# Kernel tuning notes

Measured on AMD Instinct MI355X. Metric: run time of the kernel, lower is better.

Reference implementation:

```python
import jax, jax.numpy as jnp
import numpy as np

IN_FEATS, N_HIDDEN, NUM_LAYERS, N_CLASSES, CLS_HIDDEN = 166, 76, 2, 2, 510
T, N, E = 3, 100000, 1600000
RRELU_SLOPE = (1.0 / 8.0 + 1.0 / 3.0) / 2.0  # eval-mode RReLU = leaky relu with mean slope


def setup_inputs() -> dict:
    key = jax.random.key(0)
    ks = jax.random.split(key, 24)
    d = {}
    d['feats'] = jax.random.normal(ks[0], (T, N, IN_FEATS), jnp.float32)
    d['src'] = jax.random.randint(ks[1], (T, E), 0, N, jnp.int32)
    d['dst'] = jax.random.randint(ks[2], (T, E), 0, N, jnp.int32)
    # TopK scorers (uniform +-1/sqrt(feats))
    s0 = 1.0 / np.sqrt(IN_FEATS)
    s1 = 1.0 / np.sqrt(N_HIDDEN)
    d['scorer0'] = jax.random.uniform(ks[3], (IN_FEATS, 1), jnp.float32, -s0, s0)
    d['scorer1'] = jax.random.uniform(ks[4], (N_HIDDEN, 1), jnp.float32, -s1, s1)
    # GCN weights (xavier-ish)
    d['gcn_w0'] = jax.random.normal(ks[5], (IN_FEATS, N_HIDDEN), jnp.float32) * np.sqrt(2.0 / (IN_FEATS + N_HIDDEN))
    d['gcn_w1'] = jax.random.normal(ks[6], (N_HIDDEN, N_HIDDEN), jnp.float32) * np.sqrt(2.0 / (2 * N_HIDDEN))
    # GRU params, torch layout: W_ih [3H, H_in], W_hh [3H, H], gate order (r, z, n)
    g = 1.0 / np.sqrt(N_HIDDEN)
    H3 = 3 * N_HIDDEN
    d['gru0_wih'] = jax.random.uniform(ks[7], (H3, N_HIDDEN), jnp.float32, -g, g)
    d['gru0_whh'] = jax.random.uniform(ks[8], (H3, N_HIDDEN), jnp.float32, -g, g)
    d['gru0_bih'] = jax.random.uniform(ks[9], (H3,), jnp.float32, -g, g)
    d['gru0_bhh'] = jax.random.uniform(ks[10], (H3,), jnp.float32, -g, g)
    d['gru1_wih'] = jax.random.uniform(ks[11], (H3, N_HIDDEN), jnp.float32, -g, g)
    d['gru1_whh'] = jax.random.uniform(ks[12], (H3, N_HIDDEN), jnp.float32, -g, g)
    d['gru1_bih'] = jax.random.uniform(ks[13], (H3,), jnp.float32, -g, g)
    d['gru1_bhh'] = jax.random.uniform(ks[14], (H3,), jnp.float32, -g, g)
    # MLP
    m1 = 1.0 / np.sqrt(N_HIDDEN)
    m2 = 1.0 / np.sqrt(CLS_HIDDEN)
    d['mlp_w1'] = jax.random.uniform(ks[15], (N_HIDDEN, CLS_HIDDEN), jnp.float32, -m1, m1)
    d['mlp_b1'] = jax.random.uniform(ks[16], (CLS_HIDDEN,), jnp.float32, -m1, m1)
    d['mlp_w2'] = jax.random.uniform(ks[17], (CLS_HIDDEN, N_CLASSES), jnp.float32, -m2, m2)
    d['mlp_b2'] = jax.random.uniform(ks[18], (N_CLASSES,), jnp.float32, -m2, m2)
    return d


def _topk_pool(x, scorer, k):
    # x: [N, F]; returns X_tilde: [F, k]
    scores = (x @ scorer).ravel() / jnp.linalg.norm(scorer)
    vals, idx = jax.lax.top_k(scores, k)
    out = x[idx] * jnp.tanh(vals)[:, None]  # [k, F]
    return out.T


def _gru_step(x, h, wih, whh, bih, bhh):
    # x: [B, H_in], h: [B, H]; torch GRU gate order r, z, n
    gx = x @ wih.T + bih
    gh = h @ whh.T + bhh
    H = h.shape[1]
    rx, zx, nx = gx[:, :H], gx[:, H:2 * H], gx[:, 2 * H:]
    rh, zh, nh = gh[:, :H], gh[:, H:2 * H], gh[:, 2 * H:]
    r = jax.nn.sigmoid(rx + rh)
    z = jax.nn.sigmoid(zx + zh)
    n = jnp.tanh(nx + r * nh)
    return (1.0 - z) * n + z * h


def _graph_conv(x, W, src, dst, n_nodes):
    # DGL GraphConv, norm='both', bias=False, RReLU (eval) activation
    deg_out = jnp.zeros((n_nodes,), x.dtype).at[src].add(1.0)
    deg_in = jnp.zeros((n_nodes,), x.dtype).at[dst].add(1.0)
    norm_src = jnp.clip(deg_out, 1.0, None) ** -0.5
    norm_dst = jnp.clip(deg_in, 1.0, None) ** -0.5
    h = (x * norm_src[:, None]) @ W  # project first (small out dim)
    agg = jax.ops.segment_sum(h[src], dst, num_segments=n_nodes)
    out = agg * norm_dst[:, None]
    return jnp.where(out >= 0, out, out * RRELU_SLOPE)


def reference(feats, src, dst, scorer0, scorer1, gcn_w0, gcn_w1,
              gru0_wih, gru0_whh, gru0_bih, gru0_bhh,
              gru1_wih, gru1_whh, gru1_bih, gru1_bhh,
              mlp_w1, mlp_b1, mlp_w2, mlp_b2):
    scorers = [scorer0, scorer1]
    gcn_ws = [gcn_w0, gcn_w1]
    grus = [(gru0_wih, gru0_whh, gru0_bih, gru0_bhh),
            (gru1_wih, gru1_whh, gru1_bih, gru1_bhh)]
    feat_list = [feats[t] for t in range(T)]
    for i in range(NUM_LAYERS):
        W = gcn_ws[i]
        wih, whh, bih, bhh = grus[i]
        for t in range(T):
            x_tilde = _topk_pool(feat_list[t], scorers[i], N_HIDDEN)  # [F, k]
            W = _gru_step(x_tilde, W, wih, whh, bih, bhh)  # evolve weights
            feat_list[t] = _graph_conv(feat_list[t], W, src[t], dst[t], N)
    h = feat_list[-1]
    h = jax.nn.relu(h @ mlp_w1 + mlp_b1)
    return h @ mlp_w2 + mlp_b2
```

## Files before the change

### kernel.cpp

```cpp
#include <hip/hip_runtime.h>
#include <math.h>

#define NN 100000
#define EE 1600000
#define F0 166
#define HID 76
#define H3 228
#define CHID 510
#define SLOPE 0.22916666666666666f
#define CAND_MAX 4096
#define NBIN 4096
#define HPAD 20

#define BSH 9
#define BSZ 512
#define NBKT 196
#define CH 4096
#define NCHK 391
#define NBAND 13
#define AGG_NWG 7422

__device__ __forceinline__ unsigned f2key(float f){
    unsigned u = __float_as_uint(f);
    return (u & 0x80000000u) ? ~u : (u | 0x80000000u);
}
__device__ __forceinline__ float key2f(unsigned k){
    unsigned u = (k & 0x80000000u) ? (k & 0x7fffffffu) : ~k;
    return __uint_as_float(u);
}

__global__ void scorer_norms_k(const float* __restrict__ s0, const float* __restrict__ s1,
                               float* __restrict__ outn){
    __shared__ float red[256];
    int tid = threadIdx.x;
    float a = 0.f;
    for (int k = tid; k < F0; k += 256) a += s0[k]*s0[k];
    red[tid] = a; __syncthreads();
    for (int s = 128; s > 0; s >>= 1){ if (tid < s) red[tid] += red[tid+s]; __syncthreads(); }
    if (tid == 0) outn[0] = 1.0f/sqrtf(red[0]);
    __syncthreads();
    float b = 0.f;
    for (int k = tid; k < HID; k += 256) b += s1[k]*s1[k];
    red[tid] = b; __syncthreads();
    for (int s = 128; s > 0; s >>= 1){ if (tid < s) red[tid] += red[tid+s]; __syncthreads(); }
    if (tid == 0) outn[1] = 1.0f/sqrtf(red[0]);
}

__global__ void pad_k(const float* __restrict__ w1, const float* __restrict__ b1,
                      const float* __restrict__ w2, float* __restrict__ w1t,
                      float* __restrict__ b1p, float* __restrict__ w2p){
    int idx = blockIdx.x*256 + threadIdx.x;
    if (idx < 512*HID){
        int j = idx / HID, k = idx - j*HID;
        w1t[idx] = (j < CHID) ? w1[k*CHID + j] : 0.f;
    }
    if (idx < 512)  b1p[idx] = (idx < CHID)   ? b1[idx] : 0.f;
    if (idx < 1024) w2p[idx] = (idx < CHID*2) ? w2[idx] : 0.f;
}


__global__ __launch_bounds__(256) void p1_hist_k(const int* __restrict__ src, const int* __restrict__ dst,
                                                 int* __restrict__ bhS, int* __restrict__ bhD){
    __shared__ int hS[NBKT], hD[NBKT];
    int t = blockIdx.y, blk = blockIdx.x, tid = threadIdx.x;
    for (int i = tid; i < NBKT; i += 256){ hS[i] = 0; hD[i] = 0; }
    __syncthreads();
    size_t ebase = (size_t)t*EE + (size_t)blk*CH;
    int m = EE - blk*CH; if (m > CH) m = CH;
    for (int j = tid; j < m; j += 256){
        atomicAdd(&hS[src[ebase + j] >> BSH], 1);
        atomicAdd(&hD[dst[ebase + j] >> BSH], 1);
    }
    __syncthreads();
    for (int i = tid; i < NBKT; i += 256){
        bhS[((size_t)t*NBKT + i)*NCHK + blk] = hS[i];
        bhD[((size_t)t*NBKT + i)*NCHK + blk] = hD[i];
    }
}

__global__ __launch_bounds__(512) void p2_scan_k(int* __restrict__ bhS, int* __restrict__ bhD,
                                                 int* __restrict__ ctS, int* __restrict__ ctD){
    __shared__ int sd[512];
    int b = blockIdx.x, t = blockIdx.y, tid = threadIdx.x;
    for (int a = 0; a < 2; a++){
        int* bh = a ? bhD : bhS;
        int* ct = a ? ctD : ctS;
        int* row = bh + ((size_t)t*NBKT + b)*NCHK;
        int v = (tid < NCHK) ? row[tid] : 0;
        sd[tid] = v; __syncthreads();
        for (int off = 1; off < 512; off <<= 1){
            int x = (tid >= off) ? sd[tid - off] : 0;
            __syncthreads();
            sd[tid] += x;
            __syncthreads();
        }
        if (tid < NCHK) row[tid] = sd[tid] - v;
        if (tid == 511) ct[t*NBKT + b] = sd[511];
        __syncthreads();
    }
}

__global__ __launch_bounds__(256) void p3_base_k(const int* __restrict__ ctS, const int* __restrict__ ctD,
                                                 int* __restrict__ bbS, int* __restrict__ bbD){
    __shared__ int sd[256];
    int tid = threadIdx.x;
    for (int a = 0; a < 2; a++){
        const int* ct = a ? ctD : ctS;
        int* bb = a ? bbD : bbS;
        for (int t = 0; t < 3; t++){
            int v = (tid < NBKT) ? ct[t*NBKT + tid] : 0;
            sd[tid] = v; __syncthreads();
            for (int off = 1; off < 256; off <<= 1){
                int x = (tid >= off) ? sd[tid - off] : 0;
                __syncthreads();
                sd[tid] += x;
                __syncthreads();
            }
            if (tid < NBKT) bb[t*(NBKT+1) + tid] = sd[tid] - v;
            if (tid == 0)   bb[t*(NBKT+1) + NBKT] = EE;
            __syncthreads();
        }
    }
}

__global__ __launch_bounds__(256) void p4_scatter_k(const int* __restrict__ src, const int* __restrict__ dst,
                                                    const int* __restrict__ bhS, const int* __restrict__ bhD,
                                                    const int* __restrict__ bbS, const int* __restrict__ bbD,
                                                    int* __restrict__ srcpart,
                                                    unsigned* __restrict__ pairpart){
    __shared__ int baseS[NBKT], baseD[NBKT], cS[NBKT], cD[NBKT];
    int t = blockIdx.y, blk = blockIdx.x, tid = threadIdx.x;
    for (int i = tid; i < NBKT; i += 256){
        baseS[i] = bbS[t*(NBKT+1) + i] + bhS[((size_t)t*NBKT + i)*NCHK + blk];
        baseD[i] = bbD[t*(NBKT+1) + i] + bhD[((size_t)t*NBKT + i)*NCHK + blk];
        cS[i] = 0; cD[i] = 0;
    }
    __syncthreads();
    size_t ebase = (size_t)t*EE + (size_t)blk*CH;
    int m = EE - blk*CH; if (m > CH) m = CH;
    int* sp = srcpart + (size_t)t*EE;
    unsigned* pp = pairpart + (size_t)t*EE;
    for (int j = tid; j < m; j += 256){
        int s = src[ebase + j], d = dst[ebase + j];
        int bs = s >> BSH, bd = d >> BSH;
        int r0 = atomicAdd(&cS[bs], 1);
        sp[baseS[bs] + r0] = s;
        int r1 = atomicAdd(&cD[bd], 1);
        pp[baseD[bd] + r1] = ((unsigned)s << BSH) | (unsigned)(d & (BSZ-1));
    }
}

__global__ __launch_bounds__(256) void p5_degO_k(const int* __restrict__ srcpart,
                                                 const int* __restrict__ bbS,
                                                 float* __restrict__ nO){
    __shared__ int cnt[BSZ];
    int b = blockIdx.x, t = blockIdx.y, tid = threadIdx.x;
    for (int i = tid; i < BSZ; i += 256) cnt[i] = 0;
    __syncthreads();
    int st = bbS[t*(NBKT+1) + b], en = bbS[t*(NBKT+1) + b + 1];
    const int* sp = srcpart + (size_t)t*EE;
    for (int j = st + tid; j < en; j += 256) atomicAdd(&cnt[sp[j] & (BSZ-1)], 1);
    __syncthreads();
    int nb = b << BSH;
    for (int i = tid; i < BSZ; i += 256){
        int n = nb + i;
        if (n < NN){
            int o = cnt[i]; if (o < 1) o = 1;
            nO[t*NN + n] = 1.0f/sqrtf((float)o);
        }
    }
}

__global__ __launch_bounds__(512) void p6_csr_k(const unsigned* __restrict__ pairpart,
                                                const int* __restrict__ bbD,
                                                int* __restrict__ degI, int* __restrict__ rs,
                                                float* __restrict__ nI,
                                                int* __restrict__ col){
    __shared__ int cnt2[BSZ*NBAND];
    __shared__ int fc2[BSZ*NBAND];
    __shared__ int sd[BSZ];
    int b = blockIdx.x, t = blockIdx.y, tid = threadIdx.x;
    for (int i = tid; i < BSZ*NBAND; i += 512){ cnt2[i] = 0; fc2[i] = 0; }
    __syncthreads();
    int st = bbD[t*(NBKT+1) + b], en = bbD[t*(NBKT+1) + b + 1];
    const unsigned* pp = pairpart + (size_t)t*EE;
    for (int j = st + tid; j < en; j += 512){
        unsigned p = pp[j];
        int li   = (int)(p & (BSZ-1));
        int band = (int)(p >> (BSH + 13));
        atomicAdd(&cnt2[li*NBAND + band], 1);
    }
    __syncthreads();
    int rowcnt = 0;
    #pragma unroll
    for (int bb = 0; bb < NBAND; bb++) rowcnt += cnt2[tid*NBAND + bb];
    sd[tid] = rowcnt; __syncthreads();
    for (int off = 1; off < 512; off <<= 1){
        int x = (tid >= off) ? sd[tid - off] : 0;
        __syncthreads();
        sd[tid] += x;
        __syncthreads();
    }
    int rowEx = sd[tid] - rowcnt;
    int run = rowEx;
    #pragma unroll
    for (int bb = 0; bb < NBAND; bb++){
        int cvv = cnt2[tid*NBAND + bb];
        cnt2[tid*NBAND + bb] = run;
        run += cvv;
    }
    int nb = b << BSH;
    int n = nb + tid;
    if (n < NN){
        degI[t*NN + n] = rowcnt;
        rs[t*NN + n] = st + rowEx;
        int ii = rowcnt; if (ii < 1) ii = 1;
        nI[t*NN + n] = 1.0f/sqrtf((float)ii);
    }
    __syncthreads();
    int* ct = col + (size_t)t*EE;
    for (int j = st + tid; j < en; j += 512){
        unsigned p = pp[j];
        int s  = (int)(p >> BSH);
        int li = (int)(p & (BSZ-1));
        int band = s >> 13;
        int r = atomicAdd(&fc2[li*NBAND + band], 1);
        ct[st + cnt2[li*NBAND + band] + r] = s;
    }
}


template<int F, int PAD>
__global__ __launch_bounds__(256) void score_k(const float* __restrict__ x,
                                               const float* __restrict__ scorer,
                                               const float* __restrict__ invn,
                                               float* __restrict__ scores,
                                               unsigned* hist){
    __shared__ float xs[64*PAD];
    __shared__ float part[256];
    int tid = threadIdx.x;
    int n0 = blockIdx.x*64;
    int nodes = NN - n0; if (nodes > 64) nodes = 64;
    for (int idx = tid; idx < nodes*F; idx += 256){
        int n = idx / F, k = idx - n*F;
        xs[n*PAD + k] = x[(size_t)(n0+n)*F + k];
    }
    __syncthreads();
    int w = __builtin_amdgcn_readfirstlane(tid >> 6);
    int lane = tid & 63;
    int k0 = (F*w) >> 2, k1 = (F*(w+1)) >> 2;
    const float* xrow = xs + lane*PAD;
    float s = 0.f;
    for (int k = k0; k < k1; k++) s += xrow[k]*scorer[k];
    part[w*64 + lane] = s;
    __syncthreads();
    if (tid < 64 && n0 + tid < NN){
        float tot = (part[tid] + part[64+tid] + part[128+tid] + part[192+tid]) * invn[0];
        scores[n0 + tid] = tot;
        atomicAdd(&hist[f2key(tot) >> 20], 1u);
    }
}

__global__ __launch_bounds__(256) void compact_k(const float* __restrict__ scores,
                                                 const unsigned* __restrict__ hist,
                                                 float* __restrict__ cv, int* __restrict__ ci, int* cnt){
    __shared__ unsigned cs[256];
    __shared__ int thr_s;
    int tid = threadIdx.x;
    unsigned s = 0;
    int base = NBIN - 1 - tid*16;
    for (int j = 0; j < 16; j++) s += hist[base - j];
    cs[tid] = s; __syncthreads();
    if (tid == 0){
        unsigned acc = 0; int c = 0;
        for (; c < 256; c++){ if (acc + cs[c] >= 76u) break; acc += cs[c]; }
        int b = NBIN - 1 - c*16;
        int sel = 0;
        for (int j = 0; j < 16; j++){
            acc += hist[b - j];
            if (acc >= 76u){ sel = b - j; break; }
        }
        thr_s = sel;
    }
    __syncthreads();
    int thr = thr_s;
    int n = blockIdx.x*256 + tid;
    if (n >= NN) return;
    float sv = scores[n];
    if ((int)(f2key(sv) >> 20) >= thr){
        int p = atomicAdd(cnt, 1);
        if (p < CAND_MAX){ cv[p] = sv; ci[p] = n; }
    }
}

__global__ __launch_bounds__(256) void topk_k(const float* __restrict__ cv,
                                              const int* __restrict__ ci,
                                              const int* __restrict__ cnt,
                                              int* __restrict__ topidx,
                                              float* __restrict__ tanhv){
    __shared__ unsigned long long keys[CAND_MAX];
    int tid = threadIdx.x;
    int M = *cnt; if (M > CAND_MAX) M = CAND_MAX;
    for (int i = tid; i < M; i += 256)
        keys[i] = ((unsigned long long)f2key(cv[i]) << 32) | (unsigned)(~ci[i]);
    __syncthreads();
    for (int i = tid; i < M; i += 256){
        unsigned long long ki = keys[i];
        int r = 0;
        for (int j = 0; j < M; j++) r += (keys[j] > ki) ? 1 : 0;
        if (r < 76){
            topidx[r] = (int)(~(unsigned)(ki & 0xffffffffu));
            tanhv[r]  = tanhf(key2f((unsigned)(ki >> 32)));
        }
    }
}

template<int F>
__global__ void gru_k(const float* __restrict__ cur, const int* __restrict__ topidx,
                      const float* __restrict__ tanhv, float* __restrict__ W,
                      float* __restrict__ Wt,
                      const float* __restrict__ wih, const float* __restrict__ whh,
                      const float* __restrict__ bih, const float* __restrict__ bhh){
    __shared__ float xr[HID], hr[HID], gx[H3], gh[H3];
    int r = blockIdx.x, tid = threadIdx.x;
    if (tid < HID){
        xr[tid] = cur[(size_t)topidx[tid]*F + r] * tanhv[tid];
        hr[tid] = W[r*HID + tid];
    }
    __syncthreads();
    if (tid < H3){
        const float* wi = wih + tid*HID;
        const float* wh = whh + tid*HID;
        float sa = 0.f, sb = 0.f;
        for (int k = 0; k < HID; k++){ sa += xr[k]*wi[k]; sb += hr[k]*wh[k]; }
        gx[tid] = bih[tid] + sa;
        gh[tid] = bhh[tid] + sb;
    }
    __syncthreads();
    if (tid < HID){
        float rr = 1.f/(1.f + expf(-(gx[tid] + gh[tid])));
        float zz = 1.f/(1.f + expf(-(gx[HID+tid] + gh[HID+tid])));
        float nn = tanhf(gx[2*HID+tid] + rr*gh[2*HID+tid]);
        float nv = (1.f - zz)*nn + zz*hr[tid];
        W[r*HID + tid] = nv;
        int c = tid >> 2, i = tid & 3;
        Wt[(c*F + r)*4 + i] = nv;
    }
}

template<int F, int PAD, int NB>
__global__ __launch_bounds__(256) void gemm_k(const float* __restrict__ x,
                                              const float* __restrict__ Wt,
                                              const float* __restrict__ nO,
                                              float* __restrict__ h){
    __shared__ __align__(16) float xs[NB*PAD];
    int tid = threadIdx.x;
    int n0 = blockIdx.x*NB;
    int nodes = NN - n0; if (nodes > NB) nodes = NB;
    for (int idx = tid; idx < nodes*F; idx += 256){
        int n = idx / F, k = idx - n*F;
        xs[n*PAD + k] = x[(size_t)(n0+n)*F + k];
    }
    __syncthreads();
    int w = __builtin_amdgcn_readfirstlane(tid >> 6);
    int lane = tid & 63;
    int c0 = w*5;
    const float4* Wt4 = (const float4*)Wt;
    float4 accA[5], accB[5];
    #pragma unroll
    for (int c = 0; c < 5; c++){
        accA[c] = make_float4(0.f,0.f,0.f,0.f);
        accB[c] = make_float4(0.f,0.f,0.f,0.f);
    }
    const float* xA = xs + lane*PAD;
    const float* xB = xs + ((NB==128) ? (lane+64)*PAD : lane*PAD);
    for (int k = 0; k < F; k++){
        float xa = xA[k];
        float xb = 0.f;
        if constexpr (NB == 128) xb = xB[k];
        #pragma unroll
        for (int c = 0; c < 5; c++){
            float4 wv = Wt4[(c0 + c)*F + k];
            accA[c].x += xa*wv.x; accA[c].y += xa*wv.y;
            accA[c].z += xa*wv.z; accA[c].w += xa*wv.w;
            if constexpr (NB == 128){
                accB[c].x += xb*wv.x; accB[c].y += xb*wv.y;
                accB[c].z += xb*wv.z; accB[c].w += xb*wv.w;
            }
        }
    }
    int nc = (w == 3) ? 4 : 5;
    int nA = n0 + lane;
    if (nA < NN){
        float nm = nO[nA];
        float4* h4 = (float4*)h + (size_t)nA*HPAD + c0;
        for (int c = 0; c < nc; c++){
            float4 a = accA[c];
            h4[c] = make_float4(a.x*nm, a.y*nm, a.z*nm, a.w*nm);
        }
    }
    if constexpr (NB == 128){
        int nB = n0 + 64 + lane;
        if (nB < NN){
            float nm = nO[nB];
            float4* h4 = (float4*)h + (size_t)nB*HPAD + c0;
            for (int c = 0; c < nc; c++){
                float4 a = accB[c];
                h4[c] = make_float4(a.x*nm, a.y*nm, a.z*nm, a.w*nm);
            }
        }
    }
}

__global__ __launch_bounds__(256) void agg_k(const int* __restrict__ rs, const int* __restrict__ degI,
                      const int* __restrict__ col, const float* __restrict__ h,
                      const float* __restrict__ nI, float* __restrict__ ft){
    int b0 = blockIdx.x;
    int xcd = b0 & 7, i0 = b0 >> 3;
    const int q = AGG_NWG >> 3;
    const int r8 = AGG_NWG & 7;
    int bs = (xcd < r8) ? (xcd*(q+1) + i0) : (r8*(q+1) + (xcd - r8)*q + i0);
    int idx = bs*256 + threadIdx.x;
    if (idx >= NN*19) return;
    int n = idx/19, c = idx - n*19;
    int st = rs[n], cnt = degI[n];
    const float4* h4 = (const float4*)h;
    float ax=0.f, ay=0.f, az=0.f, aw=0.f;
    int e = 0;
    for (; e + 8 <= cnt; e += 8){
        int s0 = col[st + e];
        int s1 = col[st + e + 1];
        int s2 = col[st + e + 2];
        int s3 = col[st + e + 3];
        int s4 = col[st + e + 4];
        int s5 = col[st + e + 5];
        int s6 = col[st + e + 6];
        int s7 = col[st + e + 7];
        float4 v0 = h4[(size_t)s0*HPAD + c];
        float4 v1 = h4[(size_t)s1*HPAD + c];
        float4 v2 = h4[(size_t)s2*HPAD + c];
        float4 v3 = h4[(size_t)s3*HPAD + c];
        float4 v4 = h4[(size_t)s4*HPAD + c];
        float4 v5 = h4[(size_t)s5*HPAD + c];
        float4 v6 = h4[(size_t)s6*HPAD + c];
        float4 v7 = h4[(size_t)s7*HPAD + c];
        ax += ((v0.x + v1.x) + (v2.x + v3.x)) + ((v4.x + v5.x) + (v6.x + v7.x));
        ay += ((v0.y + v1.y) + (v2.y + v3.y)) + ((v4.y + v5.y) + (v6.y + v7.y));
        az += ((v0.z + v1.z) + (v2.z + v3.z)) + ((v4.z + v5.z) + (v6.z + v7.z));
        aw += ((v0.w + v1.w) + (v2.w + v3.w)) + ((v4.w + v5.w) + (v6.w + v7.w));
    }
    for (; e + 2 <= cnt; e += 2){
        int s0 = col[st + e];
        int s1 = col[st + e + 1];
        float4 v0 = h4[(size_t)s0*HPAD + c];
        float4 v1 = h4[(size_t)s1*HPAD + c];
        ax += v0.x + v1.x; ay += v0.y + v1.y;
        az += v0.z + v1.z; aw += v0.w + v1.w;
    }
    if (e < cnt){
        int s = col[st + e];
        float4 v = h4[(size_t)s*HPAD + c];
        ax += v.x; ay += v.y; az += v.z; aw += v.w;
    }
    float nm = nI[n];
    ax*=nm; ay*=nm; az*=nm; aw*=nm;
    ax = ax >= 0.f ? ax : ax*SLOPE;
    ay = ay >= 0.f ? ay : ay*SLOPE;
    az = az >= 0.f ? az : az*SLOPE;
    aw = aw >= 0.f ? aw : aw*SLOPE;
    ((float4*)ft)[(size_t)n*19 + c] = make_float4(ax,ay,az,aw);
}

__global__ __launch_bounds__(256) void mlp4_k(const float* __restrict__ ft,
                                              const float* __restrict__ w1t,
                                              const float* __restrict__ b1p,
                                              const float* __restrict__ w2p,
                                              const float* __restrict__ b2,
                                              float* __restrict__ out){
    __shared__ __align__(16) float xs[64*HID];
    __shared__ float red[4*64*2];
    int tid = threadIdx.x;
    int n0 = blockIdx.x*64;
    {
        int rem = NN - n0; if (rem > 64) rem = 64;
        int lim = rem*19;
        const float4* g4 = (const float4*)(ft + (size_t)n0*HID);
        float4* s4 = (float4*)xs;
        for (int i = tid; i < 64*19; i += 256)
            s4[i] = (i < lim) ? g4[i] : make_float4(0.f,0.f,0.f,0.f);
    }
    __syncthreads();
    int wc = __builtin_amdgcn_readfirstlane(tid >> 6);
    int lane = tid & 63;
    int a = lane >> 3, b = lane & 7;
    const float4* xbase = (const float4*)(xs) + a*19;
    const float4* w4 = (const float4*)w1t;
    float p0[8], p1[8];
    #pragma unroll
    for (int i = 0; i < 8; i++){ p0[i] = 0.f; p1[i] = 0.f; }
    for (int jb = 0; jb < 2; jb++){
        int jbase = jb*256 + wc*64 + b;
        float acc[8][8];
        #pragma unroll
        for (int i = 0; i < 8; i++)
            #pragma unroll
            for (int m = 0; m < 8; m++) acc[i][m] = 0.f;
        const float4* wrow = w4 + jbase*19;
        for (int k4 = 0; k4 < 19; k4++){
            float4 wv[8];
            #pragma unroll
            for (int m = 0; m < 8; m++) wv[m] = wrow[m*(8*19) + k4];
            #pragma unroll
            for (int i = 0; i < 8; i++){
                float4 xv = xbase[i*(8*19) + k4];
                #pragma unroll
                for (int m = 0; m < 8; m++){
                    acc[i][m] += xv.x*wv[m].x + xv.y*wv[m].y
                               + xv.z*wv[m].z + xv.w*wv[m].w;
                }
            }
        }
        #pragma unroll
        for (int m = 0; m < 8; m++){
            int j = jbase + 8*m;
            float bias = b1p[j];
            float u0 = w2p[2*j], u1 = w2p[2*j+1];
            #pragma unroll
            for (int i = 0; i < 8; i++){
                float s = fmaxf(acc[i][m] + bias, 0.f);
                p0[i] += s*u0;
                p1[i] += s*u1;
            }
        }
    }
    #pragma unroll
    for (int off = 1; off < 8; off <<= 1){
        #pragma unroll
        for (int i = 0; i < 8; i++){
            p0[i] += __shfl_xor(p0[i], off, 64);
            p1[i] += __shfl_xor(p1[i], off, 64);
        }
    }
    if (b == 0){
        #pragma unroll
        for (int i = 0; i < 8; i++){
            int nl = a + 8*i;
            red[(wc*64 + nl)*2 + 0] = p0[i];
            red[(wc*64 + nl)*2 + 1] = p1[i];
        }
    }
    __syncthreads();
    if (tid < 128){
        int nl = tid >> 1, comp = tid & 1;
        float v = red[(0*64 + nl)*2 + comp] + red[(1*64 + nl)*2 + comp]
                + red[(2*64 + nl)*2 + comp] + red[(3*64 + nl)*2 + comp] + b2[comp];
        int n = n0 + nl;
        if (n < NN) out[(size_t)n*2 + comp] = v;
    }
}

extern "C" void kernel_launch(void* const* d_in, const int* in_sizes, int n_in,
                              void* d_out, int out_size, void* d_ws, size_t ws_size,
                              hipStream_t stream)
{
    (void)in_sizes; (void)n_in; (void)out_size; (void)ws_size;
    const float* feats   = (const float*)d_in[0];
    const int*   src     = (const int*)d_in[1];
    const int*   dst     = (const int*)d_in[2];
    const float* scorer0 = (const float*)d_in[3];
    const float* scorer1 = (const float*)d_in[4];
    const float* gcnw[2] = {(const float*)d_in[5],  (const float*)d_in[6]};
    const float* wih[2]  = {(const float*)d_in[7],  (const float*)d_in[11]};
    const float* whh[2]  = {(const float*)d_in[8],  (const float*)d_in[12]};
    const float* bih[2]  = {(const float*)d_in[9],  (const float*)d_in[13]};
    const float* bhh[2]  = {(const float*)d_in[10], (const float*)d_in[14]};
    const float* w1 = (const float*)d_in[15];
    const float* b1 = (const float*)d_in[16];
    const float* w2 = (const float*)d_in[17];
    const float* b2 = (const float*)d_in[18];
    float* out = (float*)d_out;

    char* p = (char*)d_ws;
    auto alloc = [&](size_t bytes) -> void* {
        void* r = (void*)p;
        p += (bytes + 255) & ~(size_t)255;
        return r;
    };
    float* ft[3];
    for (int t = 0; t < 3; t++) ft[t] = (float*)alloc((size_t)NN*HID*4);
    float* hbuf    = (float*)alloc((size_t)NN*HPAD*16);
    int*   col_all = (int*)alloc((size_t)3*EE*4);
    float* nO_all  = (float*)alloc((size_t)3*NN*4);
    float* nI_all  = (float*)alloc((size_t)3*NN*4);
    int*   rs_all  = (int*)alloc((size_t)3*NN*4);
    int*   dI_all  = (int*)alloc((size_t)3*NN*4);
    int* srcpart = (int*)alloc((size_t)3*EE*4);
    unsigned* pairpart = (unsigned*)alloc((size_t)3*EE*4);
    int* bhS = (int*)alloc((size_t)3*NBKT*NCHK*4);
    int* bhD = (int*)alloc((size_t)3*NBKT*NCHK*4);
    int* ctS = (int*)alloc((size_t)3*NBKT*4);
    int* ctD = (int*)alloc((size_t)3*NBKT*4);
    int* bbS = (int*)alloc((size_t)3*(NBKT+1)*4);
    int* bbD = (int*)alloc((size_t)3*(NBKT+1)*4);

    float*    scores = (float*)alloc((size_t)NN*4);
    float*    cv     = (float*)alloc(CAND_MAX*4);
    int*      ci     = (int*)alloc(CAND_MAX*4);
    int*      topidx = (int*)alloc(128*4);
    float*    tanhv  = (float*)alloc(128*4);
    float*    Wbuf   = (float*)alloc((size_t)F0*HID*4 + 256);
    float*    Wt     = (float*)alloc((size_t)19*F0*16 + 4096);
    float*    invn   = (float*)alloc(256);
    float*    w1t    = (float*)alloc((size_t)512*HID*4);
    float*    b1p    = (float*)alloc(512*4);
    float*    w2p    = (float*)alloc(1024*4);

    char* zbase = p;
    unsigned* hist6 = (unsigned*)alloc((size_t)6*NBIN*4);
    int*      ccnt6 = (int*)alloc(6*256);
    size_t zsize = (size_t)(p - zbase);

    const int gN  = (NN + 255)/256;
    const int gB  = (NN + 63)/64;
    const int gB2 = (NN + 127)/128;
    const int gP  = (512*HID + 255)/256;

    hipMemsetAsync(zbase, 0, zsize, stream);
    scorer_norms_k<<<1,256,0,stream>>>(scorer0, scorer1, invn);
    pad_k<<<gP,256,0,stream>>>(w1, b1, w2, w1t, b1p, w2p);

    p1_hist_k<<<dim3(NCHK,3),256,0,stream>>>(src, dst, bhS, bhD);
    p2_scan_k<<<dim3(NBKT,3),512,0,stream>>>(bhS, bhD, ctS, ctD);
    p3_base_k<<<1,256,0,stream>>>(ctS, ctD, bbS, bbD);
    p4_scatter_k<<<dim3(NCHK,3),256,0,stream>>>(src, dst, bhS, bhD, bbS, bbD, srcpart, pairpart);
    p5_degO_k<<<dim3(NBKT,3),256,0,stream>>>(srcpart, bbS, nO_all);
    p6_csr_k<<<dim3(NBKT,3),512,0,stream>>>(pairpart, bbD, dI_all, rs_all, nI_all, col_all);

    for (int i = 0; i < 2; i++){
        hipMemcpyAsync(Wbuf, gcnw[i], (size_t)((i==0)?F0:HID)*HID*4, hipMemcpyDeviceToDevice, stream);
        for (int t = 0; t < 3; t++){
            int q = i*3 + t;
            unsigned* hist = hist6 + (size_t)q*NBIN;
            int* ccnt = ccnt6 + q*64;
            const float* cur = (i == 0) ? (feats + (size_t)t*NN*F0) : ft[t];
            if (i == 0) score_k<F0,167><<<gB,256,0,stream>>>(cur, scorer0, invn+0, scores, hist);
            else        score_k<HID,77><<<gB,256,0,stream>>>(cur, scorer1, invn+1, scores, hist);
            compact_k<<<gN,256,0,stream>>>(scores, hist, cv, ci, ccnt);
            topk_k<<<1,256,0,stream>>>(cv, ci, ccnt, topidx, tanhv);
            if (i == 0){
                gru_k<F0><<<F0,256,0,stream>>>(cur, topidx, tanhv, Wbuf, Wt, wih[i], whh[i], bih[i], bhh[i]);
                gemm_k<F0,167,64><<<gB,256,0,stream>>>(cur, Wt, nO_all + (size_t)t*NN, hbuf);
            } else {
                gru_k<HID><<<HID,256,0,stream>>>(cur, topidx, tanhv, Wbuf, Wt, wih[i], whh[i], bih[i], bhh[i]);
                gemm_k<HID,77,128><<<gB2,256,0,stream>>>(cur, Wt, nO_all + (size_t)t*NN, hbuf);
            }
            agg_k<<<AGG_NWG,256,0,stream>>>(rs_all + (size_t)t*NN, dI_all + (size_t)t*NN,
                                            col_all + (size_t)t*EE, hbuf, nI_all + (size_t)t*NN, ft[t]);
        }
    }

    mlp4_k<<<gB,256,0,stream>>>(ft[2], w1t, b1p, w2p, b2, out);
}
```

Before: 2.518 ms.

## Restructure MLP kernel to one node per lane with wave-uniform weight rows

The final MLP kernel changes its thread mapping. Before, each lane computed an 8x8 register tile of nodes by hidden units, followed by a shuffle reduction. Now each lane keeps one node's 76-feature row in registers and loops over 128 hidden units per wave. The weight rows are read at the same address across the wave, which turns them into broadcast loads, and the cross-lane shuffle reduction goes away. The trade-off is less register-level reuse of the weights, more serial work per lane, and LDS reads of node rows at a stride of 76 floats, which may cause bank conflicts.

```diff
diff --git a/kernel.cpp b/kernel.cpp
--- a/kernel.cpp
+++ b/kernel.cpp
@@ -471,7 +471,7 @@
     ((float4*)ft)[(size_t)n*19 + c] = make_float4(ax,ay,az,aw);
 }
 
-__global__ __launch_bounds__(256) void mlp4_k(const float* __restrict__ ft,
+__global__ __launch_bounds__(256) void mlp5_k(const float* __restrict__ ft,
                                               const float* __restrict__ w1t,
                                               const float* __restrict__ b1p,
                                               const float* __restrict__ w2p,
@@ -492,63 +492,35 @@
     __syncthreads();
     int wc = __builtin_amdgcn_readfirstlane(tid >> 6);
     int lane = tid & 63;
-    int a = lane >> 3, b = lane & 7;
-    const float4* xbase = (const float4*)(xs) + a*19;
-    const float4* w4 = (const float4*)w1t;
-    float p0[8], p1[8];
-    #pragma unroll
-    for (int i = 0; i < 8; i++){ p0[i] = 0.f; p1[i] = 0.f; }
-    for (int jb = 0; jb < 2; jb++){
-        int jbase = jb*256 + wc*64 + b;
-        float acc[8][8];
+    float4 xr[19];
+    {
+        const float4* xrow = (const float4*)(xs + lane*HID);
         #pragma unroll
-        for (int i = 0; i < 8; i++)
-            #pragma unroll
-            for (int m = 0; m < 8; m++) acc[i][m] = 0.f;
-        const float4* wrow = w4 + jbase*19;
-        for (int k4 = 0; k4 < 19; k4++){
-            float4 wv[8];
-            #pragma unroll
-            for (int m = 0; m < 8; m++) wv[m] = wrow[m*(8*19) + k4];
-            #pragma unroll
-            for (int i = 0; i < 8; i++){
-                float4 xv = xbase[i*(8*19) + k4];
-                #pragma unroll
-                for (int m = 0; m < 8; m++){
-                    acc[i][m] += xv.x*wv[m].x + xv.y*wv[m].y
-                               + xv.z*wv[m].z + xv.w*wv[m].w;
-                }
-            }
-        }
+        for (int k = 0; k < 19; k++) xr[k] = xrow[k];
+    }
+    float p0 = 0.f, p1 = 0.f;
+    const int jb = wc*128;
+    const float4* wbase = (const float4*)(w1t) + (size_t)jb*19;
+    #pragma unroll 2
+    for (int jj = 0; jj < 128; jj++){
+        const float4* wr = wbase + jj*19;
+        float sx = 0.f, sy = 0.f, sz = 0.f, sw = 0.f;
         #pragma unroll
-        for (int m = 0; m < 8; m++){
-            int j = jbase + 8*m;
-            float bias = b1p[j];
-            float u0 = w2p[2*j], u1 = w2p[2*j+1];
-            #pragma unroll
-            for (int i = 0; i < 8; i++){
-                float s = fmaxf(acc[i][m] + bias, 0.f);
-                p0[i] += s*u0;
-                p1[i] += s*u1;
-            }
-        }
-    }
-    #pragma unroll
-    for (int off = 1; off < 8; off <<= 1){
-        #pragma unroll
-        for (int i = 0; i < 8; i++){
-            p0[i] += __shfl_xor(p0[i], off, 64);
-            p1[i] += __shfl_xor(p1[i], off, 64);
-        }
-    }
-    if (b == 0){
-        #pragma unroll
-        for (int i = 0; i < 8; i++){
-            int nl = a + 8*i;
-            red[(wc*64 + nl)*2 + 0] = p0[i];
-            red[(wc*64 + nl)*2 + 1] = p1[i];
-        }
-    }
+        for (int k = 0; k < 19; k++){
+            float4 w = wr[k];
+            sx += xr[k].x*w.x;
+            sy += xr[k].y*w.y;
+            sz += xr[k].z*w.z;
+            sw += xr[k].w*w.w;
+        }
+        int j = jb + jj;
+        float s = (sx + sy) + (sz + sw) + b1p[j];
+        s = fmaxf(s, 0.f);
+        p0 += s*w2p[2*j];
+        p1 += s*w2p[2*j+1];
+    }
+    red[(wc*64 + lane)*2 + 0] = p0;
+    red[(wc*64 + lane)*2 + 1] = p1;
     __syncthreads();
     if (tid < 128){
         int nl = tid >> 1, comp = tid & 1;
@@ -659,5 +631,5 @@
         }
     }
 
-    mlp4_k<<<gB,256,0,stream>>>(ft[2], w1t, b1p, w2p, b2, out);
-}
+    mlp5_k<<<gB,256,0,stream>>>(ft[2], w1t, b1p, w2p, b2, out);
+}
```

Result: slower. 2.572 ms (+2.1%).
